# Kernel tuning notes

Measured on AMD Instinct MI355X. Metric: run time of the kernel, lower is better.

Reference implementation:

```python
import jax, jax.numpy as jnp
import numpy as np

B, L, H = 2, 4096, 1024


def _rope_tables(seq_len, dim, base=10000.0):
    # standard RoPE cos/sin tables, rotate-half convention, shape [L, dim]
    inv_freq = 1.0 / (base ** (np.arange(0, dim, 2, dtype=np.float32) / dim))
    t = np.arange(seq_len, dtype=np.float32)
    freqs = np.outer(t, inv_freq)                      # [L, dim/2]
    emb = np.concatenate([freqs, freqs], axis=-1)      # [L, dim]
    return jnp.asarray(np.cos(emb)), jnp.asarray(np.sin(emb))


def setup_inputs() -> dict:
    key = jax.random.key(0)
    k1, k2 = jax.random.split(key)
    hidden_states = jax.random.normal(k1, (B, L, H), dtype=jnp.float32)
    # queries weight: normal with std = initializer_range / sqrt(2*num_layers*hidden)
    std = 0.02 / np.sqrt(2.0 * 24 * H)
    W_q = jax.random.normal(k2, (H, H), dtype=jnp.float32) * std
    cos, sin = _rope_tables(L, H)
    return {"hidden_states": hidden_states, "W_q": W_q, "cos": cos, "sin": sin}


def _rotate_half(x):
    x1, x2 = jnp.split(x, 2, axis=-1)
    return jnp.concatenate([-x2, x1], axis=-1)


def reference(hidden_states, W_q, cos, sin):
    # dropout with p=0.0 (eval) -> identity
    h = hidden_states * cos[None, :, :] + _rotate_half(hidden_states) * sin[None, :, :]  # RoPE, [B,L,H]
    q = jnp.einsum('blh,oh->blo', h, W_q)          # F.linear(h, W_q), [B,L,H]
    pre_attn = jnp.einsum('blh,bmh->blm', q, h)    # Q @ K^T (no softmax), [B,L,L]
    attention = jnp.einsum('blm,bmh->blh', pre_attn, h)  # scores @ V, [B,L,H]
    return attention
```

## Files before the change

### kernel.cpp

```cpp
#include <hip/hip_runtime.h>
#include <hip/hip_bf16.h>
#include <stdint.h>

#define BB 2
#define LL 4096
#define HH 1024
#define GBK 32

typedef __bf16 bf16;
typedef __bf16 bf16x4 __attribute__((ext_vector_type(4)));
typedef __bf16 bf16x8 __attribute__((ext_vector_type(8)));
typedef float  f32x4  __attribute__((ext_vector_type(4)));

__device__ __forceinline__ void async_cp16(const bf16* g, const bf16* l)
{
    typedef const uint32_t __attribute__((address_space(1)))* gp_t;
    typedef uint32_t __attribute__((address_space(3)))* lp_t;
    __builtin_amdgcn_global_load_lds((gp_t)(uintptr_t)g, (lp_t)(uintptr_t)l, 16, 0, 0);
}

__device__ __forceinline__ uint32_t pack_bf16(float lo, float hi)
{
    union { bf16 b; unsigned short u; } a, c;
    a.b = (bf16)lo; c.b = (bf16)hi;
    return (uint32_t)a.u | ((uint32_t)c.u << 16);
}

__global__ __launch_bounds__(256) void prep_kernel(
    const float* __restrict__ x, const float* __restrict__ cs,
    const float* __restrict__ sn, const float* __restrict__ Wq,
    bf16* __restrict__ h, bf16* __restrict__ hT, bf16* __restrict__ Wb)
{
    const int id = blockIdx.x;
    if (id >= 1024) {
        const long base = (long)(id - 1024) * 4096 + (long)threadIdx.x * 16;
#pragma unroll
        for (int j = 0; j < 4; ++j) {
            const float4 v = *(const float4*)(Wq + base + j * 4);
            bf16x4 o;
            o[0] = (bf16)v.x; o[1] = (bf16)v.y; o[2] = (bf16)v.z; o[3] = (bf16)v.w;
            *(bf16x4*)(Wb + base + j * 4) = o;
        }
        return;
    }
    __shared__ uint32_t lds[2][64][36];
    const int b  = id >> 9;
    const int v  = id & 511;
    const int r0 = (v >> 3) * 64;
    const int c0 = (v & 7) * 64;
    const int t  = threadIdx.x;
    const int c8 = t & 7;
    const int rr = t >> 3;
    const int ca = c0 + c8 * 8;
    const long xrow0 = ((long)b * LL + r0 + 2 * rr) * HH;
    const long crow0 = (long)(r0 + 2 * rr) * HH;

    float oA[2][8], oB[2][8];
#pragma unroll
    for (int rw = 0; rw < 2; ++rw) {
        const long xr = xrow0 + (long)rw * HH;
        const long cr = crow0 + (long)rw * HH;
        float xA[8], xB[8], cA[8], cB[8], sA[8], sB[8];
        *(float4*)&xA[0] = *(const float4*)(x + xr + ca);
        *(float4*)&xA[4] = *(const float4*)(x + xr + ca + 4);
        *(float4*)&xB[0] = *(const float4*)(x + xr + ca + 512);
        *(float4*)&xB[4] = *(const float4*)(x + xr + ca + 516);
        *(float4*)&cA[0] = *(const float4*)(cs + cr + ca);
        *(float4*)&cA[4] = *(const float4*)(cs + cr + ca + 4);
        *(float4*)&cB[0] = *(const float4*)(cs + cr + ca + 512);
        *(float4*)&cB[4] = *(const float4*)(cs + cr + ca + 516);
        *(float4*)&sA[0] = *(const float4*)(sn + cr + ca);
        *(float4*)&sA[4] = *(const float4*)(sn + cr + ca + 4);
        *(float4*)&sB[0] = *(const float4*)(sn + cr + ca + 512);
        *(float4*)&sB[4] = *(const float4*)(sn + cr + ca + 516);
#pragma unroll
        for (int j = 0; j < 8; ++j) {
            oA[rw][j] = xA[j] * cA[j] - xB[j] * sA[j];
            oB[rw][j] = xB[j] * cB[j] + xA[j] * sB[j];
        }
        bf16x8 hA, hB;
#pragma unroll
        for (int j = 0; j < 8; ++j) { hA[j] = (bf16)oA[rw][j]; hB[j] = (bf16)oB[rw][j]; }
        *(bf16x8*)(h + xr + ca)       = hA;
        *(bf16x8*)(h + xr + ca + 512) = hB;
    }
#pragma unroll
    for (int j = 0; j < 8; ++j) {
        lds[0][c8 * 8 + j][rr] = pack_bf16(oA[0][j], oA[1][j]);
        lds[1][c8 * 8 + j][rr] = pack_bf16(oB[0][j], oB[1][j]);
    }
    __syncthreads();

    const int cc = t >> 2;
    const int q  = t & 3;
#pragma unroll
    for (int s = 0; s < 2; ++s) {
        const int hrow = (s ? c0 + 512 : c0) + cc;
        bf16* po = hT + (long)b * HH * LL + (long)hrow * LL + r0 + q * 16;
        const uint4 w0 = *(const uint4*)&lds[s][cc][q * 8];
        const uint4 w1 = *(const uint4*)&lds[s][cc][q * 8 + 4];
        *(uint4*)(po)     = w0;
        *(uint4*)(po + 8) = w1;
    }
}

__global__ __launch_bounds__(128) void rope_kernel(
    const float* __restrict__ x, const float* __restrict__ cs,
    const float* __restrict__ sn, bf16* __restrict__ h)
{
    const int l = blockIdx.x;
    const int b = blockIdx.y;
    const int i = threadIdx.x * 4;
    const long xb = ((long)b * LL + l) * HH;
    const long cb = (long)l * HH;
    const float4 x1 = *(const float4*)(x + xb + i);
    const float4 x2 = *(const float4*)(x + xb + i + HH / 2);
    const float4 c1 = *(const float4*)(cs + cb + i);
    const float4 c2 = *(const float4*)(cs + cb + i + HH / 2);
    const float4 s1 = *(const float4*)(sn + cb + i);
    const float4 s2 = *(const float4*)(sn + cb + i + HH / 2);
    bf16x4 o1, o2;
    o1[0] = (bf16)(x1.x * c1.x - x2.x * s1.x);
    o1[1] = (bf16)(x1.y * c1.y - x2.y * s1.y);
    o1[2] = (bf16)(x1.z * c1.z - x2.z * s1.z);
    o1[3] = (bf16)(x1.w * c1.w - x2.w * s1.w);
    o2[0] = (bf16)(x2.x * c2.x + x1.x * s2.x);
    o2[1] = (bf16)(x2.y * c2.y + x1.y * s2.y);
    o2[2] = (bf16)(x2.z * c2.z + x1.z * s2.z);
    o2[3] = (bf16)(x2.w * c2.w + x1.w * s2.w);
    *(bf16x4*)(h + xb + i)          = o1;
    *(bf16x4*)(h + xb + i + HH / 2) = o2;
}

__global__ __launch_bounds__(256) void transpose_bf16_64(
    const bf16* __restrict__ in, bf16* __restrict__ out, const int R, const int C)
{
    __shared__ uint32_t lds[64][36];
    const long zoff = (long)blockIdx.z * R * C;
    const int r0 = blockIdx.x * 64;
    const int c0 = blockIdx.y * 64;
    const int t  = threadIdx.x;
    const int c8 = t & 7;
    const int rr = t >> 3;
    const bf16* p0 = in + zoff + (long)(r0 + 2 * rr) * C + c0 + c8 * 8;
    const uint4 ra = *(const uint4*)p0;
    const uint4 rb = *(const uint4*)(p0 + C);
    const uint32_t av[4] = {ra.x, ra.y, ra.z, ra.w};
    const uint32_t bv[4] = {rb.x, rb.y, rb.z, rb.w};
#pragma unroll
    for (int j = 0; j < 4; ++j) {
        const uint32_t alo = av[j] & 0xffffu, ahi = av[j] >> 16;
        const uint32_t blo = bv[j] & 0xffffu, bhi = bv[j] >> 16;
        lds[c8 * 8 + 2 * j    ][rr] = alo | (blo << 16);
        lds[c8 * 8 + 2 * j + 1][rr] = ahi | (bhi << 16);
    }
    __syncthreads();
    const int c = t >> 2;
    const int q = t & 3;
    const uint4 w0 = *(const uint4*)&lds[c][q * 8];
    const uint4 w1 = *(const uint4*)&lds[c][q * 8 + 4];
    bf16* po = out + zoff + (long)(c0 + c) * R + r0 + q * 16;
    *(uint4*)(po)     = w0;
    *(uint4*)(po + 8) = w1;
}

__global__ __launch_bounds__(256) void cast_wq(
    const float* __restrict__ Wq, bf16* __restrict__ Wb)
{
    const long idx = ((long)blockIdx.x * 256 + threadIdx.x) * 4;
    const float4 v = *(const float4*)(Wq + idx);
    bf16x4 o;
    o[0] = (bf16)v.x; o[1] = (bf16)v.y; o[2] = (bf16)v.z; o[3] = (bf16)v.w;
    *(bf16x4*)(Wb + idx) = o;
}

#define GEMM_SHARED()                                                          \
    __shared__ __align__(16) bf16 As_[2][128][32];                             \
    __shared__ __align__(16) bf16 Bs_[2][128][32];

#define GEMM_PREFETCH(KOFF, BUF)                                               \
    do {                                                                       \
        async_cp16(Ag + (KOFF),           &As_[BUF][0][0] + woff0);            \
        async_cp16(Ag + (KOFF) + 64L * K, &As_[BUF][0][0] + woff1);            \
        async_cp16(Bg + (KOFF),           &Bs_[BUF][0][0] + woff0);            \
        async_cp16(Bg + (KOFF) + 64L * K, &Bs_[BUF][0][0] + woff1);            \
    } while (0)

#define GEMM_BODY(M0, N0, KBASE, KEND, DST, DT, LDN)                           \
    {                                                                          \
        const int tid  = threadIdx.x;                                          \
        const int lane = tid & 63;                                             \
        const int wave = tid >> 6;                                             \
        const int wm = (wave & 1) * 64;                                        \
        const int wn = (wave >> 1) * 64;                                       \
        const int fr = lane & 15;                                              \
        const int fq = lane >> 4;                                              \
        const int srow = tid >> 2;                                             \
        const int scol = (tid & 3) * 8;                                        \
        const int woff0 = wave * 512;                                          \
        const int woff1 = 2048 + wave * 512;                                   \
        const bf16* Ag = Ab + (long)((M0) + srow) * K + scol;                  \
        const bf16* Bg = Bb + (long)((N0) + srow) * K + scol;                  \
        const f32x4 vzero = {0.f, 0.f, 0.f, 0.f};                              \
        f32x4 acc[4][4];                                                       \
        _Pragma("unroll") for (int i = 0; i < 4; ++i)                          \
            _Pragma("unroll") for (int j = 0; j < 4; ++j) acc[i][j] = vzero;   \
        GEMM_PREFETCH(KBASE, 0);                                               \
        int buf = 0;                                                           \
        for (int k0 = (KBASE); k0 < (KEND); k0 += GBK, buf ^= 1) {             \
            __syncthreads();                                                   \
            if (k0 + GBK < (KEND)) GEMM_PREFETCH(k0 + GBK, buf ^ 1);           \
            bf16x8 af[4], bfv[4];                                              \
            _Pragma("unroll") for (int i = 0; i < 4; ++i)                      \
                af[i]  = *(const bf16x8*)&As_[buf][wm + i * 16 + fr][fq * 8];  \
            _Pragma("unroll") for (int j = 0; j < 4; ++j)                      \
                bfv[j] = *(const bf16x8*)&Bs_[buf][wn + j * 16 + fr][fq * 8];  \
            _Pragma("unroll") for (int i = 0; i < 4; ++i)                      \
                _Pragma("unroll") for (int j = 0; j < 4; ++j)                  \
                    acc[i][j] = __builtin_amdgcn_mfma_f32_16x16x32_bf16(       \
                        af[i], bfv[j], acc[i][j], 0, 0, 0);                    \
        }                                                                      \
        _Pragma("unroll") for (int i = 0; i < 4; ++i) {                        \
            _Pragma("unroll") for (int r = 0; r < 4; ++r) {                    \
                const int row = (M0) + wm + i * 16 + fq * 4 + r;               \
                _Pragma("unroll") for (int j = 0; j < 4; ++j) {                \
                    const int col = (N0) + wn + j * 16 + fr;                   \
                    (DST)[(long)row * (LDN) + col] = (DT)acc[i][j][r];         \
                }                                                              \
            }                                                                  \
        }                                                                      \
    }

template <typename OUT_T>
__global__ __launch_bounds__(256) void gemm_bt(
    const bf16* __restrict__ A, const bf16* __restrict__ B, OUT_T* __restrict__ C,
    const int M, const int N, const int K,
    const long sA, const long sB, const long sC)
{
    GEMM_SHARED();
    const bf16* Ab = A + blockIdx.z * sA;
    const bf16* Bb = B + blockIdx.z * sB;
    OUT_T*      Cb = C + blockIdx.z * sC;
    const int m0 = blockIdx.x * 128;
    const int n0 = blockIdx.y * 128;
    GEMM_BODY(m0, n0, 0, K, Cb, OUT_T, N);
}

#define E_STAGE_A(KT, PART, BUF)                                               \
  do {                                                                         \
    const int kk0_ = kbase + (KT) * 64;                                        \
    _Pragma("unroll") for (int qq_ = 0; qq_ < 2; ++qq_) {                      \
      const int ch_  = qq_ * 512 + tid;                                        \
      const int sl_  = ch_ >> 3;                                               \
      const int cc_  = (ch_ & 7) ^ (sl_ & 7);                                  \
      const int row_ = (sl_ & 63) + (PART) * 64 + ((sl_ >> 6) << 7);           \
      async_cp16(Ab + (long)(m0 + row_) * K + kk0_ + cc_ * 8,                  \
                 &As[BUF][PART][0][0] + (qq_ * 512 + (tid & 448)) * 8);        \
    }                                                                          \
  } while (0)

#define E_STAGE_B(KT, PART, BUF)                                               \
  do {                                                                         \
    const int kk0_ = kbase + (KT) * 64;                                        \
    _Pragma("unroll") for (int qq_ = 0; qq_ < 2; ++qq_) {                      \
      const int ch_  = qq_ * 512 + tid;                                        \
      const int sl_  = ch_ >> 3;                                               \
      const int cc_  = (ch_ & 7) ^ (sl_ & 7);                                  \
      const int row_ = (sl_ & 31) + (PART) * 32 + ((sl_ >> 5) << 6);           \
      async_cp16(Bb + (long)(n0 + row_) * K + kk0_ + cc_ * 8,                  \
                 &Bs[BUF][PART][0][0] + (qq_ * 512 + (tid & 448)) * 8);        \
    }                                                                          \
  } while (0)

#define E_STAGE_B2(KT, PART, BUF)                                              \
  do {                                                                         \
    const int kk0_ = kbase + (KT) * 64;                                        \
    const int sl_  = tid >> 3;                                                 \
    const int cc_  = (tid & 7) ^ (sl_ & 7);                                    \
    const int row_ = (sl_ & 15) + (PART) * 16 + ((sl_ >> 4) << 5);             \
    async_cp16(Bb + (long)(n0 + row_) * K + kk0_ + cc_ * 8,                    \
               &Bs2[BUF][PART][0][0] + (tid & 448) * 8);                       \
  } while (0)

#define E_LOAD_A(BUF, IG)                                                      \
  do {                                                                         \
    const bf16* Ap_ = &As[BUF][IG][0][0] + (wr * 64 + fr) * 64;                \
    _Pragma("unroll") for (int ii_ = 0; ii_ < 4; ++ii_)                        \
      _Pragma("unroll") for (int kk_ = 0; kk_ < 2; ++kk_)                      \
        af[ii_][kk_] = *(const bf16x8*)(Ap_ + ii_ * 1024 +                     \
                        (((kk_ * 4 + fq) ^ fr7) * 8));                         \
  } while (0)

#define E_LOAD_Bv(BUF, JP, DSTV)                                               \
  do {                                                                         \
    const bf16* Bp_ = &Bs[BUF][JP][0][0] + (wc * 32 + fr) * 64;                \
    _Pragma("unroll") for (int jj_ = 0; jj_ < 2; ++jj_)                        \
      _Pragma("unroll") for (int kk_ = 0; kk_ < 2; ++kk_)                      \
        DSTV[jj_][kk_] = *(const bf16x8*)(Bp_ + jj_ * 1024 +                   \
                        (((kk_ * 4 + fq) ^ fr7) * 8));                         \
  } while (0)

#define E_LOAD_B2(BUF, JG, DSTV)                                               \
  do {                                                                         \
    const bf16* Bp_ = &Bs2[BUF][JG][0][0] + (wc * 16 + fr) * 64;               \
    _Pragma("unroll") for (int kk_ = 0; kk_ < 2; ++kk_)                        \
      DSTV[kk_] = *(const bf16x8*)(Bp_ + (((kk_ * 4 + fq) ^ fr7) * 8));        \
  } while (0)

#define E_MMA(IG, JG, BV)                                                      \
  do {                                                                         \
    __builtin_amdgcn_s_setprio(1);                                             \
    _Pragma("unroll") for (int ii_ = 0; ii_ < 4; ++ii_)                        \
      _Pragma("unroll") for (int jj_ = 0; jj_ < 2; ++jj_)                      \
        _Pragma("unroll") for (int kk_ = 0; kk_ < 2; ++kk_)                    \
          acc[(IG) * 4 + ii_][(JG) * 2 + jj_] =                                \
              __builtin_amdgcn_mfma_f32_16x16x32_bf16(                         \
                  af[ii_][kk_], BV[jj_][kk_],                                  \
                  acc[(IG) * 4 + ii_][(JG) * 2 + jj_], 0, 0, 0);               \
    __builtin_amdgcn_s_setprio(0);                                             \
  } while (0)

#define E_MMA2(IG, JG, BV)                                                     \
  do {                                                                         \
    __builtin_amdgcn_s_setprio(1);                                             \
    _Pragma("unroll") for (int ii_ = 0; ii_ < 4; ++ii_)                        \
      _Pragma("unroll") for (int kk_ = 0; kk_ < 2; ++kk_)                      \
        acc2[(IG) * 4 + ii_][JG] =                                             \
            __builtin_amdgcn_mfma_f32_16x16x32_bf16(                           \
                af[ii_][kk_], BV[kk_], acc2[(IG) * 4 + ii_][JG], 0, 0, 0);     \
    __builtin_amdgcn_s_setprio(0);                                             \
  } while (0)

#define E_BAR()   __builtin_amdgcn_s_barrier()
#define E_LGKM0() do { asm volatile("s_waitcnt lgkmcnt(0)" ::: "memory");      \
                       __builtin_amdgcn_sched_barrier(0); } while (0)
#define E_VM(N)   asm volatile("s_waitcnt vmcnt(" #N ")" ::: "memory")

#define E_COMMON_IDX()                                                         \
  const int tid  = threadIdx.x;                                                \
  const int lane = tid & 63;                                                   \
  const int wv   = tid >> 6;                                                   \
  const int wr   = wv >> 2;                                                    \
  const int wc   = wv & 3;                                                     \
  const int fr   = lane & 15;                                                  \
  const int fq   = lane >> 4;                                                  \
  const int fr7  = fr & 7;                                                     \
  (void)lane;

__global__ __launch_bounds__(512, 2) void gemm8_Gq(
    const bf16* __restrict__ hT, const bf16* __restrict__ Wb,
    const bf16* __restrict__ h, float* __restrict__ P, bf16* __restrict__ q)
{
    __shared__ __align__(16) bf16 As[2][2][128][64];
    __shared__ __align__(16) bf16 Bs[2][2][128][64];
    E_COMMON_IDX();
    bf16x8 af[4][2], bfv0[2][2], bfv1[2][2];
    f32x4 acc[8][4];
#pragma unroll
    for (int i_ = 0; i_ < 8; ++i_)
#pragma unroll
        for (int j_ = 0; j_ < 4; ++j_) acc[i_][j_] = (f32x4){0.f, 0.f, 0.f, 0.f};

    const int id = blockIdx.x;
    const bf16* Ab; const bf16* Bb;
    int K, kbase, m0, n0;
    float* Pc = nullptr;
    if (id < 128) {
        m0 = (id & 31) * 256;
        n0 = (id >> 5) * 256;
        Ab = h; Bb = Wb; K = HH; kbase = 0;
    } else {
        const int u  = id - 128;
        const int zb = u >> 6;
        const int v  = u & 63;
        const int zs = v >> 4;
        const int tl = v & 15;
        m0 = (tl & 3) * 256;
        n0 = (tl >> 2) * 256;
        Ab = hT + (long)zb * HH * LL; Bb = Ab;
        K  = LL; kbase = zs * (LL / 4);
        Pc = P + (long)(zb * 4 + zs) * HH * HH;
    }

    E_STAGE_A(0, 0, 0); E_STAGE_B(0, 1, 0); E_STAGE_A(0, 1, 0);
    E_STAGE_B(0, 0, 0);
    E_STAGE_A(1, 0, 1); E_STAGE_B(1, 1, 1); E_STAGE_A(1, 1, 1);
    E_VM(6); E_BAR();
    int t_ = 0;
#pragma unroll 1
    for (; t_ + 3 < 16; t_ += 2) {
         E_LOAD_A(0, 0); E_LOAD_Bv(0, 0, bfv0); E_STAGE_B(t_ + 1, 0, 1);
                 E_BAR(); E_LGKM0(); E_MMA(0, 0, bfv0); E_BAR();
         E_LOAD_Bv(0, 1, bfv1); E_STAGE_A(t_ + 2, 0, 0);
                 E_BAR(); E_LGKM0(); E_MMA(0, 1, bfv1); E_BAR();
         E_LOAD_A(0, 1); E_STAGE_B(t_ + 2, 1, 0);
                 E_BAR(); E_LGKM0(); E_MMA(1, 1, bfv1); E_BAR();
         E_STAGE_A(t_ + 2, 1, 0);
                 E_MMA(1, 0, bfv0); E_VM(6); E_BAR();
         E_LOAD_A(1, 0); E_LOAD_Bv(1, 0, bfv0); E_STAGE_B(t_ + 2, 0, 0);
                 E_BAR(); E_LGKM0(); E_MMA(0, 0, bfv0); E_BAR();
         E_LOAD_Bv(1, 1, bfv1); E_STAGE_A(t_ + 3, 0, 1);
                 E_BAR(); E_LGKM0(); E_MMA(0, 1, bfv1); E_BAR();
         E_LOAD_A(1, 1); E_STAGE_B(t_ + 3, 1, 1);
                 E_BAR(); E_LGKM0(); E_MMA(1, 1, bfv1); E_BAR();
         E_STAGE_A(t_ + 3, 1, 1);
                 E_MMA(1, 0, bfv0); E_VM(6); E_BAR();
    }
    E_LOAD_A(0, 0); E_LOAD_Bv(0, 0, bfv0); E_STAGE_B(t_ + 1, 0, 1);
    E_BAR(); E_LGKM0(); E_MMA(0, 0, bfv0); E_BAR();
    E_LOAD_Bv(0, 1, bfv1); E_BAR(); E_LGKM0(); E_MMA(0, 1, bfv1); E_BAR();
    E_LOAD_A(0, 1); E_BAR(); E_LGKM0(); E_MMA(1, 1, bfv1); E_BAR();
    E_MMA(1, 0, bfv0); E_VM(0); E_BAR();
    E_LOAD_A(1, 0); E_LOAD_Bv(1, 0, bfv0); E_BAR(); E_LGKM0(); E_MMA(0, 0, bfv0); E_BAR();
    E_LOAD_Bv(1, 1, bfv1); E_BAR(); E_LGKM0(); E_MMA(0, 1, bfv1); E_BAR();
    E_LOAD_A(1, 1); E_BAR(); E_LGKM0(); E_MMA(1, 1, bfv1); E_BAR();
    E_MMA(1, 0, bfv0);

    if (Pc) {
#pragma unroll
        for (int gi = 0; gi < 8; ++gi)
#pragma unroll
            for (int r = 0; r < 4; ++r) {
                const int row = m0 + wr * 128 + gi * 16 + fq * 4 + r;
#pragma unroll
                for (int gj = 0; gj < 4; ++gj)
                    Pc[(long)row * HH + n0 + wc * 64 + gj * 16 + fr] = acc[gi][gj][r];
            }
    } else {
#pragma unroll
        for (int gi = 0; gi < 8; ++gi)
#pragma unroll
            for (int r = 0; r < 4; ++r) {
                const int row = m0 + wr * 128 + gi * 16 + fq * 4 + r;
#pragma unroll
                for (int gj = 0; gj < 4; ++gj)
                    q[(long)row * HH + n0 + wc * 64 + gj * 16 + fr] = (bf16)acc[gi][gj][r];
            }
    }
}

__global__ __launch_bounds__(512, 2) void gemm8_qG(
    const bf16* __restrict__ qm, const bf16* __restrict__ G, float* __restrict__ out)
{
    __shared__ __align__(16) bf16 As[2][2][128][64];
    __shared__ __align__(16) bf16 Bs2[2][2][64][64];
    E_COMMON_IDX();
    bf16x8 af[4][2], bw0[2], bw1[2];
    f32x4 acc2[8][2];
#pragma unroll
    for (int i_ = 0; i_ < 8; ++i_)
#pragma unroll
        for (int j_ = 0; j_ < 2; ++j_) acc2[i_][j_] = (f32x4){0.f, 0.f, 0.f, 0.f};

    const int id = blockIdx.x;
    const int b  = id >> 7;
    const int u  = id & 127;
    const int m0 = (u & 15) * 256;
    const int n0 = (u >> 4) * 128;
    const bf16* Ab = qm + (long)b * LL * HH;
    const bf16* Bb = G + (long)b * HH * HH;
    const int K = HH, kbase = 0;
    float* outb = out + (long)b * LL * HH;

    E_STAGE_A(0, 0, 0); E_STAGE_B2(0, 1, 0); E_STAGE_A(0, 1, 0);
    E_STAGE_B2(0, 0, 0);
    E_STAGE_A(1, 0, 1); E_STAGE_B2(1, 1, 1); E_STAGE_A(1, 1, 1);
    E_VM(5); E_BAR();
    int t_ = 0;
#pragma unroll 1
    for (; t_ + 3 < 16; t_ += 2) {
         E_LOAD_A(0, 0); E_LOAD_B2(0, 0, bw0); E_STAGE_B2(t_ + 1, 0, 1);
                 E_BAR(); E_LGKM0(); E_MMA2(0, 0, bw0); E_BAR();
         E_LOAD_B2(0, 1, bw1); E_STAGE_A(t_ + 2, 0, 0);
                 E_BAR(); E_LGKM0(); E_MMA2(0, 1, bw1); E_BAR();
         E_LOAD_A(0, 1); E_STAGE_B2(t_ + 2, 1, 0);
                 E_BAR(); E_LGKM0(); E_MMA2(1, 1, bw1); E_BAR();
         E_STAGE_A(t_ + 2, 1, 0);
                 E_MMA2(1, 0, bw0); E_VM(5); E_BAR();
         E_LOAD_A(1, 0); E_LOAD_B2(1, 0, bw0); E_STAGE_B2(t_ + 2, 0, 0);
                 E_BAR(); E_LGKM0(); E_MMA2(0, 0, bw0); E_BAR();
         E_LOAD_B2(1, 1, bw1); E_STAGE_A(t_ + 3, 0, 1);
                 E_BAR(); E_LGKM0(); E_MMA2(0, 1, bw1); E_BAR();
         E_LOAD_A(1, 1); E_STAGE_B2(t_ + 3, 1, 1);
                 E_BAR(); E_LGKM0(); E_MMA2(1, 1, bw1); E_BAR();
         E_STAGE_A(t_ + 3, 1, 1);
                 E_MMA2(1, 0, bw0); E_VM(5); E_BAR();
    }
    E_LOAD_A(0, 0); E_LOAD_B2(0, 0, bw0); E_STAGE_B2(t_ + 1, 0, 1);
    E_BAR(); E_LGKM0(); E_MMA2(0, 0, bw0); E_BAR();
    E_LOAD_B2(0, 1, bw1); E_BAR(); E_LGKM0(); E_MMA2(0, 1, bw1); E_BAR();
    E_LOAD_A(0, 1); E_BAR(); E_LGKM0(); E_MMA2(1, 1, bw1); E_BAR();
    E_MMA2(1, 0, bw0); E_VM(0); E_BAR();
    E_LOAD_A(1, 0); E_LOAD_B2(1, 0, bw0); E_BAR(); E_LGKM0(); E_MMA2(0, 0, bw0); E_BAR();
    E_LOAD_B2(1, 1, bw1); E_BAR(); E_LGKM0(); E_MMA2(0, 1, bw1); E_BAR();
    E_LOAD_A(1, 1); E_BAR(); E_LGKM0(); E_MMA2(1, 1, bw1); E_BAR();
    E_MMA2(1, 0, bw0);

#pragma unroll
    for (int gi = 0; gi < 8; ++gi)
#pragma unroll
        for (int r = 0; r < 4; ++r) {
            const int row = m0 + wr * 128 + gi * 16 + fq * 4 + r;
#pragma unroll
            for (int gj = 0; gj < 2; ++gj)
                outb[(long)row * HH + n0 + wc * 32 + gj * 16 + fr] = acc2[gi][gj][r];
        }
}

__global__ __launch_bounds__(256) void reduce_splits(
    const float* __restrict__ P, bf16* __restrict__ out, const int npb, const int S)
{
    const int b = blockIdx.y;
    const long r = ((long)blockIdx.x * 256 + threadIdx.x) * 4;
    const float* base = P + (long)b * S * npb + r;
    float4 a = *(const float4*)(base);
    for (int s = 1; s < S; ++s) {
        const float4 v = *(const float4*)(base + (long)s * npb);
        a.x += v.x; a.y += v.y; a.z += v.z; a.w += v.w;
    }
    bf16x4 o;
    o[0] = (bf16)a.x; o[1] = (bf16)a.y; o[2] = (bf16)a.z; o[3] = (bf16)a.w;
    *(bf16x4*)(out + (long)b * npb + r) = o;
}

extern "C" void kernel_launch(void* const* d_in, const int* in_sizes, int n_in,
                              void* d_out, int out_size, void* d_ws, size_t ws_size,
                              hipStream_t stream)
{
    const float* x  = (const float*)d_in[0];
    const float* Wq = (const float*)d_in[1];
    const float* cs = (const float*)d_in[2];
    const float* sn = (const float*)d_in[3];
    float* out = (float*)d_out;
    char* ws = (char*)d_ws;

    bf16*  h  = (bf16*)(ws);
    bf16*  hT = (bf16*)(ws + 16u * 1024 * 1024);
    bf16*  Wb = (bf16*)(ws + 32u * 1024 * 1024);
    bf16*  G  = (bf16*)(ws + 34u * 1024 * 1024);
    float* P  = (float*)(ws + 38u * 1024 * 1024);

    const bool big_ws = ws_size >= (size_t)90 * 1024 * 1024;
    bf16* q = big_ws ? (bf16*)(ws + 70u * 1024 * 1024)
                     : (bf16*)(ws + 38u * 1024 * 1024);

    if (big_ws) {
        prep_kernel<<<dim3(1280), 256, 0, stream>>>(x, cs, sn, Wq, h, hT, Wb);
        gemm8_Gq<<<dim3(256), 512, 0, stream>>>(hT, Wb, h, P, q);
        reduce_splits<<<dim3(HH * HH / 1024, BB), 256, 0, stream>>>(P, G, HH * HH, 4);
        gemm8_qG<<<dim3(256), 512, 0, stream>>>(q, G, out);
    } else {
        rope_kernel<<<dim3(LL, BB), 128, 0, stream>>>(x, cs, sn, h);
        transpose_bf16_64<<<dim3(LL / 64, HH / 64, BB), 256, 0, stream>>>(h, hT, LL, HH);
        cast_wq<<<dim3(HH * HH / 1024), 256, 0, stream>>>(Wq, Wb);
        gemm_bt<bf16><<<dim3(HH / 128, HH / 128, BB), 256, 0, stream>>>(
            hT, hT, G, HH, HH, LL, (long)HH * LL, (long)HH * LL, (long)HH * HH);
        gemm_bt<bf16><<<dim3(LL / 128, HH / 128, BB), 256, 0, stream>>>(
            h, Wb, q, LL, HH, HH, (long)LL * HH, 0L, (long)LL * HH);
        gemm_bt<float><<<dim3(LL / 128, HH / 128, BB), 256, 0, stream>>>(
            q, G, out, LL, HH, HH, (long)LL * HH, (long)HH * HH, (long)LL * HH);
    }
}
```

Baseline: 182.6 us.

## Remap GEMM block ids for XCD-local L2 reuse and dedupe RoPE table loads

Both GEMM kernels now permute blockIdx so that consecutive logical tiles land on the same XCD (bid&7 picks the XCD slot). The tile order is also rearranged so that blocks sharing A rows or B panels run on one XCD, which should raise L2 hit rates on the chiplet design. The RoPE pre-kernel also drops the second-half cos/sin loads and reuses the first-half values, since the tables are duplicated across halves. That saves global memory traffic but depends on that duplicated table structure.

```diff
diff --git a/kernel.cpp b/kernel.cpp
--- a/kernel.cpp
+++ b/kernel.cpp
@@ -60,23 +60,19 @@
     for (int rw = 0; rw < 2; ++rw) {
         const long xr = xrow0 + (long)rw * HH;
         const long cr = crow0 + (long)rw * HH;
-        float xA[8], xB[8], cA[8], cB[8], sA[8], sB[8];
+        float xA[8], xB[8], cA[8], sA[8];
         *(float4*)&xA[0] = *(const float4*)(x + xr + ca);
         *(float4*)&xA[4] = *(const float4*)(x + xr + ca + 4);
         *(float4*)&xB[0] = *(const float4*)(x + xr + ca + 512);
         *(float4*)&xB[4] = *(const float4*)(x + xr + ca + 516);
         *(float4*)&cA[0] = *(const float4*)(cs + cr + ca);
         *(float4*)&cA[4] = *(const float4*)(cs + cr + ca + 4);
-        *(float4*)&cB[0] = *(const float4*)(cs + cr + ca + 512);
-        *(float4*)&cB[4] = *(const float4*)(cs + cr + ca + 516);
         *(float4*)&sA[0] = *(const float4*)(sn + cr + ca);
         *(float4*)&sA[4] = *(const float4*)(sn + cr + ca + 4);
-        *(float4*)&sB[0] = *(const float4*)(sn + cr + ca + 512);
-        *(float4*)&sB[4] = *(const float4*)(sn + cr + ca + 516);
 #pragma unroll
         for (int j = 0; j < 8; ++j) {
             oA[rw][j] = xA[j] * cA[j] - xB[j] * sA[j];
-            oB[rw][j] = xB[j] * cB[j] + xA[j] * sB[j];
+            oB[rw][j] = xB[j] * cA[j] + xA[j] * sA[j];
         }
         bf16x8 hA, hB;
 #pragma unroll
@@ -361,25 +357,26 @@
 #pragma unroll
         for (int j_ = 0; j_ < 4; ++j_) acc[i_][j_] = (f32x4){0.f, 0.f, 0.f, 0.f};
 
-    const int id = blockIdx.x;
+    const int bid = blockIdx.x;
+    const int id  = (bid & 7) * 32 + (bid >> 3);
     const bf16* Ab; const bf16* Bb;
     int K, kbase, m0, n0;
     float* Pc = nullptr;
     if (id < 128) {
-        m0 = (id & 31) * 256;
-        n0 = (id >> 5) * 256;
+        m0 = (id >> 2) * 256;
+        n0 = (id & 3) * 256;
         Ab = h; Bb = Wb; K = HH; kbase = 0;
     } else {
         const int u  = id - 128;
-        const int zb = u >> 6;
-        const int v  = u & 63;
-        const int zs = v >> 4;
-        const int tl = v & 15;
+        const int pl = u >> 4;
+        const int zb = pl >> 2;
+        const int zs = pl & 3;
+        const int tl = u & 15;
         m0 = (tl & 3) * 256;
         n0 = (tl >> 2) * 256;
         Ab = hT + (long)zb * HH * LL; Bb = Ab;
         K  = LL; kbase = zs * (LL / 4);
-        Pc = P + (long)(zb * 4 + zs) * HH * HH;
+        Pc = P + (long)pl * HH * HH;
     }
 
     E_STAGE_A(0, 0, 0); E_STAGE_B(0, 1, 0); E_STAGE_A(0, 1, 0);
@@ -452,11 +449,12 @@
 #pragma unroll
         for (int j_ = 0; j_ < 2; ++j_) acc2[i_][j_] = (f32x4){0.f, 0.f, 0.f, 0.f};
 
-    const int id = blockIdx.x;
-    const int b  = id >> 7;
-    const int u  = id & 127;
-    const int m0 = (u & 15) * 256;
-    const int n0 = (u >> 4) * 128;
+    const int bid = blockIdx.x;
+    const int id  = (bid & 7) * 32 + (bid >> 3);
+    const int mb  = id >> 3;
+    const int b   = mb >> 4;
+    const int m0  = (mb & 15) * 256;
+    const int n0  = (id & 7) * 128;
     const bf16* Ab = qm + (long)b * LL * HH;
     const bf16* Bb = G + (long)b * HH * HH;
     const int K = HH, kbase = 0;
```

After: 179.2 us. Within noise of the previous version (-1.8%).
